# Performance work log

Hardware: AMD Instinct MI355X
Metric: run time of the kernel (lower is better)

The kernel has to match this reference:

```python
import jax, jax.numpy as jnp
import numpy as np
import math

GAMMA = 0.9
H = 8
SCALE_BASE = 512
TWO_PI = 2.0 * math.pi


def fixed_pos_embedding(scale):
    # scale: (L, d2) ; returns sin, cos of shape (L, d2)
    L, d2 = scale.shape
    inv_freq = 1.0 / (10000.0 ** (jnp.arange(d2, dtype=jnp.float32) / d2))
    sinusoid = jnp.arange(L, dtype=jnp.float32)[:, None] * inv_freq[None, :]
    return jnp.sin(sinusoid), jnp.cos(sinusoid)


def duplicate_interleave(m):
    # (L, d2) -> (L, 2*d2), each element duplicated along last axis
    return jnp.repeat(m, 2, axis=1)


def rotate_every_two(x):
    x1 = x[..., 0::2]
    x2 = x[..., 1::2]
    return jnp.stack([-x2, x1], axis=-1).reshape(x.shape)


def xpos(x, downscale=False):
    # x: (B, L, D) ; xpos rotary scaling (RetNet style, head_dim = D)
    B, L, D = x.shape
    base = (jnp.arange(0, D, 2, dtype=jnp.float32) + 0.4 * D) / (1.4 * D)  # (D/2,)
    power = (jnp.arange(L, dtype=jnp.float32) / SCALE_BASE)[:, None]       # (L, 1)
    scale = base[None, :] ** power                                          # (L, D/2)
    sin, cos = fixed_pos_embedding(scale)
    if downscale:
        scale = 1.0 / scale
    sin = duplicate_interleave(sin * scale)  # (L, D)
    cos = duplicate_interleave(cos * scale)  # (L, D)
    return x * cos[None] + rotate_every_two(x) * sin[None]


def pos_embed_sine(x, mask):
    # 1D DETR-style sine positional embedding. x: (B, L, D), mask: (1, L)
    D = x.shape[-1]
    x_embed = jnp.cumsum(mask, axis=1)
    x_embed = x_embed / (x_embed[:, -1:] + 1e-6) * TWO_PI
    dim_t = jnp.arange(D, dtype=jnp.float32)
    dim_t = 10000.0 ** (2.0 * jnp.floor(dim_t / 2.0) / D)
    pos = x_embed[:, :, None] / dim_t                       # (1, L, D)
    pos = jnp.stack([jnp.sin(pos[:, :, 0::2]), jnp.cos(pos[:, :, 1::2])], axis=3)
    return pos.reshape(1, x.shape[1], D)


def _split_heads(x):
    # (B, S, D) -> (B*H, S, d_k), matching torch view(S, B*H, d_k).transpose(0,1)
    B, S, D = x.shape
    return x.transpose(1, 0, 2).reshape(S, B * H, D // H).transpose(1, 0, 2)


def _forward(src, W_txt_Q, W_txt_K, W_txt_V, W_vid_Q, W_vid_K, W_vid_V,
             learn_vid_ret, W_out, b_out, row_idx, col_idx, txt_len):
    B, S, Dm = src.shape
    vid_len = S - txt_len
    dk = Dm // H
    # retention decay matrix D (lower triangular gamma^(n-m))
    n = jnp.arange(S)[:, None]
    m = jnp.arange(S)[None, :]
    expo = jnp.where(n >= m, n - m, 0).astype(jnp.float32)
    Dmat = jnp.where(n >= m, GAMMA ** expo, 0.0)
    # learned sparse mask: gather-expanded (vid_len,vid_len) table -> (S,S)
    temp = learn_vid_ret.reshape(vid_len, vid_len)
    learn_ret = jax.nn.sigmoid(temp[row_idx, col_idx])  # (S, S)
    diag = jnp.eye(S, dtype=src.dtype)
    video_ret = (1.0 - diag) * learn_ret
    learn_mask = diag + video_ret
    mask = Dmat * learn_mask   # mask_mode='both'
    loss_sparsity = jnp.mean(jnp.abs(video_ret))
    # projections (att_mode='all')
    txt = src[:, :txt_len]
    vid = src[:, txt_len:]
    mask_txt = jnp.ones((1, txt_len), dtype=src.dtype)
    pos = pos_embed_sine(txt, mask_txt)
    txt_Q = (pos + txt) @ W_txt_Q
    txt_K = (pos + txt) @ W_txt_K
    txt_V = txt @ W_txt_V
    vid_Q = xpos(vid) @ W_vid_Q
    vid_K = xpos(vid, downscale=True) @ W_vid_K
    vid_V = vid @ W_vid_V
    Q = jnp.concatenate([txt_Q, vid_Q], axis=1)
    K = jnp.concatenate([txt_K, vid_K], axis=1)
    V = jnp.concatenate([txt_V, vid_V], axis=1)
    q = _split_heads(Q) / math.sqrt(dk)   # (B*H, S, dk)
    k = _split_heads(K)
    v = _split_heads(V)
    attn = jnp.einsum('bqd,bkd->bqk', q, k) * mask[None]  # multiplicative mask pre-softmax
    attn = jax.nn.softmax(attn, axis=-1)
    ctx = jnp.einsum('bqk,bkd->bqd', attn, v)             # (B*H, S, dk)
    ctx = ctx.transpose(1, 0, 2).reshape(S, B, Dm)
    out = ctx @ W_out.T + b_out                            # output Linear
    out = out.transpose(1, 0, 2)                           # (B, S, Dm)
    att = attn.reshape(B, H, S, S).sum(axis=1) / H
    return out, att, loss_sparsity


def setup_inputs() -> dict:
    key = jax.random.key(0)
    ks = jax.random.split(key, 12)
    B, S, Dm, txt_len = 16, 1056, 256, 32
    vid_len = S - txt_len
    inp = {
        'src': jax.random.normal(ks[0], (B, S, Dm), dtype=jnp.float32),
        'W_txt_Q': jax.random.normal(ks[1], (Dm, Dm), dtype=jnp.float32) / Dm,
        'W_txt_K': jax.random.normal(ks[2], (Dm, Dm), dtype=jnp.float32) / Dm,
        'W_txt_V': jax.random.normal(ks[3], (Dm, Dm), dtype=jnp.float32) / Dm,
        'W_vid_Q': jax.random.normal(ks[4], (Dm, Dm), dtype=jnp.float32) / Dm,
        'W_vid_K': jax.random.normal(ks[5], (Dm, Dm), dtype=jnp.float32) / Dm,
        'W_vid_V': jax.random.normal(ks[6], (Dm, Dm), dtype=jnp.float32) / Dm,
        'learn_vid_ret': jax.random.normal(ks[7], (vid_len * vid_len, 1), dtype=jnp.float32),
        'W_out': jax.random.normal(ks[8], (Dm, Dm), dtype=jnp.float32) / math.sqrt(Dm),
        'b_out': jnp.zeros((Dm,), dtype=jnp.float32),
        'row_idx': jax.random.randint(ks[9], (S, S), 0, vid_len, dtype=jnp.int32),
        'col_idx': jax.random.randint(ks[10], (S, S), 0, vid_len, dtype=jnp.int32),
        'txt_len': txt_len,
    }
    return inp


def reference(src, W_txt_Q, W_txt_K, W_txt_V, W_vid_Q, W_vid_K, W_vid_V,
              learn_vid_ret, W_out, b_out, row_idx, col_idx, txt_len):
    return _forward(src, W_txt_Q, W_txt_K, W_txt_V, W_vid_Q, W_vid_K, W_vid_V,
                    learn_vid_ret, W_out, b_out, row_idx, col_idx, txt_len)
```

## Files before the change

kernel.cpp:

```cpp
#include <hip/hip_runtime.h>
#include <math.h>

#define B_   16
#define S_   1056
#define DM_  256
#define H_   8
#define DK_  32
#define TXT_ 32
#define VID_ 1024
#define SS_  (S_*S_)
#define NQT_ 66
#define NKT_ 66
#define MASK_BLKS 1089

#define LOG2_10000f 13.28771237954945f
#define LOG2_GAMMAf (-0.15200309344504995f)
#define RSQRT_DKf   0.17677669529663687f
#define TWO_PIf     6.283185307179586f
#define LOG2Ef      1.4426950408889634f

typedef __attribute__((ext_vector_type(8))) short bf16x8;
typedef __attribute__((ext_vector_type(4))) short bf16x4;
typedef __attribute__((ext_vector_type(4))) float f32x4;

__device__ __forceinline__ short f2bf(float f){
    unsigned u = __float_as_uint(f);
    unsigned r = u + 0x7FFFu + ((u >> 16) & 1u);
    return (short)(r >> 16);
}
__device__ __forceinline__ float bf2f(unsigned short s){
    return __uint_as_float(((unsigned)s) << 16);
}
__device__ __forceinline__ float fexp2(float x){
#if __has_builtin(__builtin_amdgcn_exp2f)
    return __builtin_amdgcn_exp2f(x);
#else
    return exp2f(x);
#endif
}
__device__ __forceinline__ bf16x4 pack_bf16x4(float e0, float e1, float e2, float e3){
    unsigned w0, w1;
    asm("v_cvt_pk_bf16_f32 %0, %1, %2" : "=v"(w0) : "v"(e0), "v"(e1));
    asm("v_cvt_pk_bf16_f32 %0, %1, %2" : "=v"(w1) : "v"(e2), "v"(e3));
    uint2 u = make_uint2(w0, w1);
    return *(bf16x4*)&u;
}

__device__ __forceinline__ f32x4 mfma16(bf16x4 a, bf16x4 b, f32x4 c){
#if __has_builtin(__builtin_amdgcn_mfma_f32_16x16x16bf16_1k)
    return __builtin_amdgcn_mfma_f32_16x16x16bf16_1k(a, b, c, 0, 0, 0);
#else
    f32x4 d = c;
    asm("v_mfma_f32_16x16x16_bf16 %0, %1, %2, %0" : "+v"(d) : "v"(a), "v"(b));
    return d;
#endif
}

__global__ __launch_bounds__(256) void k_mask(const float* __restrict__ lvr,
                       const int* __restrict__ row_idx, const int* __restrict__ col_idx,
                       short* __restrict__ maskf, float* __restrict__ partials)
{
    int T  = blockIdx.x*256 + threadIdx.x;
    int l  = T & 63;
    int qk = T >> 6;
    int qt = qk / 66;
    int kt = qk - qt*66;
    int i  = qt*16 + (l & 15);
    int j0 = kt*16 + 4*(l >> 4);
    size_t idx = (size_t)i*S_ + j0;
    int4 ri4 = *(const int4*)&row_idx[idx];
    int4 ci4 = *(const int4*)&col_idx[idx];
    int rr[4] = {ri4.x, ri4.y, ri4.z, ri4.w};
    int cc[4] = {ci4.x, ci4.y, ci4.z, ci4.w};
    float vrs = 0.f;
    short4 mq;
    short* mp = (short*)&mq;
    #pragma unroll
    for (int jj = 0; jj < 4; ++jj) {
        int j = j0 + jj;
        float vr, lm;
        if (i == j) { vr = 0.f; lm = 1.f; }
        else {
            float t = lvr[(size_t)rr[jj]*VID_ + cc[jj]];
            float sg = 1.f/(1.f + expf(-t));
            vr = sg; lm = sg;
        }
        float dmat = (i >= j) ? exp2f((float)(i-j)*LOG2_GAMMAf) : 0.f;
        mp[jj] = f2bf(dmat * lm * LOG2Ef);
        vrs += vr;
    }
    *(short4*)&maskf[(size_t)qk*256 + l*4] = mq;

    float s = vrs;
    #pragma unroll
    for (int m=1; m<64; m<<=1) s += __shfl_xor(s, m, 64);
    __shared__ float ws4[4];
    if ((threadIdx.x & 63) == 0) ws4[threadIdx.x>>6] = s;
    __syncthreads();
    if (threadIdx.x == 0) partials[blockIdx.x] = ws4[0]+ws4[1]+ws4[2]+ws4[3];
}

__global__ __launch_bounds__(256) void k_loss(const float* __restrict__ partials,
                                              float* __restrict__ out_loss)
{
    float s = 0.f;
    for (int i = threadIdx.x; i < MASK_BLKS; i += 256) s += partials[i];
    #pragma unroll
    for (int m=1; m<64; m<<=1) s += __shfl_xor(s, m, 64);
    __shared__ float ws4[4];
    if ((threadIdx.x & 63) == 0) ws4[threadIdx.x>>6] = s;
    __syncthreads();
    if (threadIdx.x == 0) out_loss[0] = (ws4[0]+ws4[1]+ws4[2]+ws4[3]) * (1.f/(float)SS_);
}

__global__ __launch_bounds__(256) void k_wprep(
    const float* __restrict__ Wtq, const float* __restrict__ Wtk, const float* __restrict__ Wtv,
    const float* __restrict__ Wvq, const float* __restrict__ Wvk, const float* __restrict__ Wvv,
    const float* __restrict__ Wout, short* __restrict__ Wf, short* __restrict__ WoF)
{
    int seg = blockIdx.x >> 8;
    int r   = blockIdx.x & 255;
    int tid = threadIdx.x;
    int tb16 = r >> 4, lr = r & 15;
    int kk = tid >> 5, lg = (tid >> 3) & 3, j = tid & 7;
    size_t off = (((size_t)tb16*8 + kk) << 9) + (lr + 16*lg)*8 + j;
    if (seg == 6) {
        WoF[off] = f2bf(Wout[r*256 + tid]);
    } else {
        const float* Wsrc = seg==0?Wtq: seg==1?Wtk: seg==2?Wtv: seg==3?Wvq: seg==4?Wvk: Wvv;
        Wf[((size_t)seg << 16) + off] = f2bf(Wsrc[tid*256 + r]);
    }
}

__global__ __launch_bounds__(256, 2) void k_qkv(const float* __restrict__ src,
    const short* __restrict__ WFq, const short* __restrict__ WFk, const short* __restrict__ WFv,
    short* __restrict__ Qb, short* __restrict__ Kf, short* __restrict__ Vf, int is_txt)
{
    __shared__ __align__(16) short xb[3][16][256];
    __shared__ float invf[128];
    __shared__ float lbs[128];
    int tid = threadIdx.x;
    int r0 = blockIdx.x * 16;
    int b, srow0;
    if (is_txt) { b = r0 >> 5;  srow0 = r0 & 31; }
    else        { b = r0 >> 10; srow0 = TXT_ + (r0 & 1023); }
    int t16 = srow0 >> 4;

    if (tid < 128) {
        float fk = (float)tid;
        invf[tid] = exp2f(-fk*(1.f/128.f)*LOG2_10000f);
        lbs[tid]  = log2f((2.f*fk + 102.4f) * (1.f/358.4f));
    }
    __syncthreads();

    #pragma unroll
    for (int it = 0; it < 8; ++it) {
        int task = it*256 + tid;
        int k  = task >> 4;
        int rr = task & 15;
        int srow = srow0 + rr;
        float2 x01 = ((const float2*)(src + ((size_t)b*S_ + srow)*DM_))[k];
        float a0, a1, c0, c1;
        if (is_txt) {
            float xe  = (float)(srow + 1) * (TWO_PIf/(32.f + 1e-6f));
            float arg = xe * invf[k];
            float sn = __sinf(arg), cs = __cosf(arg);
            a0 = x01.x + sn; a1 = x01.y + cs;
            c0 = a0; c1 = a1;
        } else {
            int l = srow - TXT_;
            float arg = (float)l * invf[k];
            float sn = __sinf(arg), cs = __cosf(arg);
            float scale = exp2f((float)l*(1.f/512.f)*lbs[k]);
            float rsc = 1.f/scale;
            float y0 = x01.x*cs - x01.y*sn;
            float y1 = x01.y*cs + x01.x*sn;
            a0 = y0*scale; a1 = y1*scale;
            c0 = y0*rsc;   c1 = y1*rsc;
        }
        int col = (2*k) ^ ((rr&7)<<3);
        *(short2*)&xb[0][rr][col] = make_short2(f2bf(a0), f2bf(a1));
        *(short2*)&xb[1][rr][col] = make_short2(f2bf(c0), f2bf(c1));
        *(short2*)&xb[2][rr][col] = make_short2(f2bf(x01.x), f2bf(x01.y));
    }
    __syncthreads();

    int lane = tid & 63;
    int w    = tid >> 6;
    int lr   = lane & 15;
    int lg   = lane >> 4;
    int swzl = (lr & 7) << 3;

    const short* WFs[3] = {WFq, WFk, WFv};
    #pragma unroll
    for (int m = 0; m < 3; ++m) {
        bf16x8 xf[8];
        #pragma unroll
        for (int kk = 0; kk < 8; ++kk)
            xf[kk] = *(const bf16x8*)&xb[m][lr][(kk*32 + lg*8) ^ swzl];
        #pragma unroll
        for (int ct = 0; ct < 4; ++ct) {
            int tb16 = w + ct*4;
            int tb   = tb16 * 16;
            const short* Wp = WFs[m] + (((size_t)tb16*8) << 9) + lane*8;
            f32x4 acc = {0.f,0.f,0.f,0.f};
            if (m < 2) {
                #pragma unroll
                for (int kk = 0; kk < 8; ++kk) {
                    bf16x8 wf = *(const bf16x8*)(Wp + (kk << 9));
                    acc = __builtin_amdgcn_mfma_f32_16x16x32_bf16(wf, xf[kk], acc, 0, 0, 0);
                }
                int h  = tb >> 5;
                int d0 = (tb & 31) + lg*4;
                short4 s4;
                if (m == 0) {
                    s4.x=f2bf(acc[0]*RSQRT_DKf); s4.y=f2bf(acc[1]*RSQRT_DKf);
                    s4.z=f2bf(acc[2]*RSQRT_DKf); s4.w=f2bf(acc[3]*RSQRT_DKf);
                    size_t off = ((size_t)(b*H_+h)*S_ + srow0+lr)*DK_ + d0;
                    *(short4*)&Qb[off] = s4;
                } else {
                    s4.x=f2bf(acc[0]); s4.y=f2bf(acc[1]);
                    s4.z=f2bf(acc[2]); s4.w=f2bf(acc[3]);
                    int lK = lr + 16*(d0 >> 3);
                    *(short4*)&Kf[((((size_t)(b*H_+h)*NKT_ + t16) << 9)) + lK*8 + (d0 & 7)] = s4;
                }
            } else {
                #pragma unroll
                for (int kk = 0; kk < 8; ++kk) {
                    bf16x8 wf = *(const bf16x8*)(Wp + (kk << 9));
                    acc = __builtin_amdgcn_mfma_f32_16x16x32_bf16(xf[kk], wf, acc, 0, 0, 0);
                }
                int o = tb + lr;
                int h = o >> 5;
                int dh = (tb >> 4) & 1;
                short4 s4;
                s4.x=f2bf(acc[0]); s4.y=f2bf(acc[1]);
                s4.z=f2bf(acc[2]); s4.w=f2bf(acc[3]);
                *(short4*)&Vf[((((size_t)(b*H_+h)*NKT_ + t16)) << 9) + lane*8 + dh*4] = s4;
            }
        }
    }
}

#define CTX_TILE2(KF, M0V, M1V, VV)                                               \
    {                                                                             \
        f32x4 acc0 = {0.f,0.f,0.f,0.f};                                           \
        acc0 = __builtin_amdgcn_mfma_f32_16x16x32_bf16(KF, qf0, acc0, 0, 0, 0);   \
        f32x4 acc1 = {0.f,0.f,0.f,0.f};                                           \
        acc1 = __builtin_amdgcn_mfma_f32_16x16x32_bf16(KF, qf1, acc1, 0, 0, 0);   \
        float e0 = fexp2(acc0[0]*bf2f(M0V.x));                                    \
        float e1 = fexp2(acc0[1]*bf2f(M0V.y));                                    \
        float e2 = fexp2(acc0[2]*bf2f(M0V.z));                                    \
        float e3 = fexp2(acc0[3]*bf2f(M0V.w));                                    \
        rssum0 += (e0+e1) + (e2+e3);                                              \
        bf16x4 pb0 = pack_bf16x4(e0, e1, e2, e3);                                 \
        float f0 = fexp2(acc1[0]*bf2f(M1V.x));                                    \
        float f1 = fexp2(acc1[1]*bf2f(M1V.y));                                    \
        float f2 = fexp2(acc1[2]*bf2f(M1V.z));                                    \
        float f3 = fexp2(acc1[3]*bf2f(M1V.w));                                    \
        rssum1 += (f0+f1) + (f2+f3);                                              \
        bf16x4 pb1 = pack_bf16x4(f0, f1, f2, f3);                                 \
        bf16x4 vlo; vlo[0]=VV[0]; vlo[1]=VV[1]; vlo[2]=VV[2]; vlo[3]=VV[3];       \
        bf16x4 vhi; vhi[0]=VV[4]; vhi[1]=VV[5]; vhi[2]=VV[6]; vhi[3]=VV[7];       \
        pv00 = mfma16(pb0, vlo, pv00);                                            \
        pv01 = mfma16(pb0, vhi, pv01);                                            \
        pv10 = mfma16(pb1, vlo, pv10);                                            \
        pv11 = mfma16(pb1, vhi, pv11);                                            \
    }

__global__ __launch_bounds__(256, 4) void k_ctx(const short* __restrict__ Qb,
    const short* __restrict__ Kf, const short* __restrict__ Vf,
    const short* __restrict__ maskf, short* __restrict__ ctxf, float* __restrict__ denomG)
{
    int tid  = threadIdx.x;
    int lane = tid & 63;
    int w    = tid >> 6;
    int b    = blockIdx.x & 15;
    int qh   = blockIdx.x >> 4;
    int qt32 = qh >> 1;
    int head = (qh & 1)*4 + w;
    int q0   = qt32 * 32;
    int lr   = lane & 15;
    int lg   = lane >> 4;

    const int bh = b*H_ + head;
    bf16x8 qf0 = *(const bf16x8*)(Qb + ((size_t)bh*S_ + q0 + lr)*DK_ + lg*8);
    bf16x8 qf1 = *(const bf16x8*)(Qb + ((size_t)bh*S_ + q0 + 16 + lr)*DK_ + lg*8);
    const short* Kp  = Kf + (((size_t)bh*NKT_) << 9) + lane*8;
    const short* Vp  = Vf + (((size_t)bh*NKT_) << 9) + lane*8;
    const short* Mp0 = maskf + (((size_t)(qt32*2  )*NKT_) << 8) + lane*4;
    const short* Mp1 = maskf + (((size_t)(qt32*2+1)*NKT_) << 8) + lane*4;

    float rssum0 = 0.f, rssum1 = 0.f;
    f32x4 pv00 = {0.f,0.f,0.f,0.f}, pv01 = {0.f,0.f,0.f,0.f};
    f32x4 pv10 = {0.f,0.f,0.f,0.f}, pv11 = {0.f,0.f,0.f,0.f};

    for (int g = 0; g < 22; ++g) {
        int tb = g * 3;
        bf16x8 K[3], VV[3]; ushort4 M0[3], M1[3];
        #pragma unroll
        for (int c = 0; c < 3; ++c) {
            int t = tb + c;
            K[c]  = *(const bf16x8*)(Kp + (unsigned)t*512);
            VV[c] = *(const bf16x8*)(Vp + (unsigned)t*512);
            M0[c] = *(const ushort4*)(Mp0 + (unsigned)t*256);
            M1[c] = *(const ushort4*)(Mp1 + (unsigned)t*256);
        }
        #pragma unroll
        for (int c = 0; c < 3; ++c) {
            CTX_TILE2(K[c], M0[c], M1[c], VV[c])
        }
    }

    rssum0 += __shfl_xor(rssum0, 16, 64);
    rssum0 += __shfl_xor(rssum0, 32, 64);
    rssum1 += __shfl_xor(rssum1, 16, 64);
    rssum1 += __shfl_xor(rssum1, 32, 64);
    float rd0 = 1.f / rssum0;
    float rd1 = 1.f / rssum1;
    if (lane < 16) {
        denomG[(size_t)bh*S_ + q0 + lane]      = rd0;
        denomG[(size_t)bh*S_ + q0 + 16 + lane] = rd1;
    }

    size_t baseA = ((((size_t)b*NQT_ + qt32*2    )*8 + head) << 9);
    size_t baseB = ((((size_t)b*NQT_ + qt32*2 + 1)*8 + head) << 9);
    int j   = lr & 7;
    int lgl = lr >> 3;
    #pragma unroll
    for (int r = 0; r < 4; ++r) {
        float rdq0 = __shfl(rd0, 4*lg + r, 64);
        float rdq1 = __shfl(rd1, 4*lg + r, 64);
        int qm = 4*lg + r;
        ctxf[baseA + (qm + 16*lgl    )*8 + j] = f2bf(pv00[r] * rdq0);
        ctxf[baseA + (qm + 16*(2+lgl))*8 + j] = f2bf(pv01[r] * rdq0);
        ctxf[baseB + (qm + 16*lgl    )*8 + j] = f2bf(pv10[r] * rdq1);
        ctxf[baseB + (qm + 16*(2+lgl))*8 + j] = f2bf(pv11[r] * rdq1);
    }
}

__global__ __launch_bounds__(256, 4) void k_att(const short* __restrict__ Qb,
    const short* __restrict__ Kf, const short* __restrict__ maskf,
    const float* __restrict__ denomG, float* __restrict__ att)
{
    int tid  = threadIdx.x;
    int lane = tid & 63;
    int w    = tid >> 6;
    int b    = blockIdx.x & 15;
    int qt   = blockIdx.x >> 4;
    int q0   = qt * 16;
    int lr   = lane & 15;
    int lg   = lane >> 4;

    float rdv[8];
    #pragma unroll
    for (int h = 0; h < 8; ++h)
        rdv[h] = denomG[(size_t)(b*H_+h)*S_ + q0 + lr] * 0.125f;

    bf16x8 qf[8];
    #pragma unroll
    for (int h = 0; h < 8; ++h)
        qf[h] = *(const bf16x8*)(Qb + ((size_t)(b*H_+h)*S_ + q0+lr)*DK_ + lg*8);

    int nt = (w < 2) ? 17 : 16;
    for (int t = 0; t < nt; ++t) {
        int kt = t*4 + w;
        int k0 = kt*16;
        bf16x8 kf[8];
        #pragma unroll
        for (int h = 0; h < 8; ++h)
            kf[h] = *(const bf16x8*)(Kf + (((size_t)(b*H_+h)*NKT_ + kt) << 9) + lane*8);
        ushort4 mq = *(const ushort4*)(maskf + (((size_t)qt*NKT_ + kt) << 8) + lane*4);
        float m0 = bf2f(mq.x), m1 = bf2f(mq.y), m2 = bf2f(mq.z), m3 = bf2f(mq.w);
        f32x4 a = {0.f,0.f,0.f,0.f};
        #pragma unroll
        for (int h = 0; h < 8; ++h) {
            f32x4 s = {0.f,0.f,0.f,0.f};
            s = __builtin_amdgcn_mfma_f32_16x16x32_bf16(kf[h], qf[h], s, 0, 0, 0);
            a[0] = fmaf(fexp2(s[0]*m0), rdv[h], a[0]);
            a[1] = fmaf(fexp2(s[1]*m1), rdv[h], a[1]);
            a[2] = fmaf(fexp2(s[2]*m2), rdv[h], a[2]);
            a[3] = fmaf(fexp2(s[3]*m3), rdv[h], a[3]);
        }
        float4 o4 = make_float4(a[0], a[1], a[2], a[3]);
        *(float4*)&att[((size_t)b*S_ + q0+lr)*S_ + k0 + 4*lg] = o4;
    }
}

__global__ __launch_bounds__(256, 2) void k_outproj(const short* __restrict__ ctxf,
    const short* __restrict__ WoF, const float* __restrict__ bias, float* __restrict__ out)
{
    int tid  = threadIdx.x;
    int lane = tid & 63;
    int w    = tid >> 6;
    int lr   = lane & 15;
    int lg   = lane >> 4;
    int r0   = blockIdx.x * 16;

    bf16x8 cf[8];
    #pragma unroll
    for (int kk = 0; kk < 8; ++kk)
        cf[kk] = *(const bf16x8*)(ctxf + (((size_t)blockIdx.x*8 + kk) << 9) + lane*8);

    #pragma unroll
    for (int ct = 0; ct < 4; ++ct) {
        int tb16 = w + ct*4;
        int tb   = tb16 * 16;
        f32x4 acc = {0.f,0.f,0.f,0.f};
        #pragma unroll
        for (int kk = 0; kk < 8; ++kk) {
            bf16x8 wf = *(const bf16x8*)(WoF + (((size_t)tb16*8 + kk) << 9) + lane*8);
            acc = __builtin_amdgcn_mfma_f32_16x16x32_bf16(wf, cf[kk], acc, 0, 0, 0);
        }
        float4 b4 = *(const float4*)&bias[tb + lg*4];
        float4 o4 = make_float4(acc[0]+b4.x, acc[1]+b4.y, acc[2]+b4.z, acc[3]+b4.w);
        *(float4*)&out[(size_t)(r0+lr)*DM_ + tb + lg*4] = o4;
    }
}

extern "C" void kernel_launch(void* const* d_in, const int* in_sizes, int n_in,
                              void* d_out, int out_size, void* d_ws, size_t ws_size,
                              hipStream_t stream)
{
    (void)in_sizes; (void)n_in; (void)out_size; (void)ws_size;
    const float* src  = (const float*)d_in[0];
    const float* Wtq  = (const float*)d_in[1];
    const float* Wtk  = (const float*)d_in[2];
    const float* Wtv  = (const float*)d_in[3];
    const float* Wvq  = (const float*)d_in[4];
    const float* Wvk  = (const float*)d_in[5];
    const float* Wvv  = (const float*)d_in[6];
    const float* lvr  = (const float*)d_in[7];
    const float* Wout = (const float*)d_in[8];
    const float* bout = (const float*)d_in[9];
    const int*   rid  = (const int*)d_in[10];
    const int*   cid  = (const int*)d_in[11];

    const size_t QKV_SH = (size_t)B_*H_*S_*DK_;
    const size_t KF_SH  = (size_t)B_*H_*NKT_*512;
    const size_t VF_SH  = (size_t)B_*H_*NKT_*512;
    const size_t CTX_SH = (size_t)B_*S_*DM_;

    float* ws       = (float*)d_ws;
    float* partials = ws;
    float* denomG   = partials + MASK_BLKS;
    short* maskf    = (short*)(denomG + (size_t)B_*H_*S_);
    short* Qb       = maskf + SS_;
    short* Kf       = Qb + QKV_SH;
    short* Vf       = Kf + KF_SH;
    short* ctxf     = Vf + VF_SH;
    short* Wf       = ctxf + CTX_SH;
    short* WoF      = Wf + 6*65536;

    float* out  = (float*)d_out;
    float* att  = out + (size_t)B_*S_*DM_;
    float* loss = att + (size_t)B_*S_*S_;

    k_mask<<<MASK_BLKS, 256, 0, stream>>>(lvr, rid, cid, maskf, partials);
    k_wprep<<<7*256, 256, 0, stream>>>(Wtq, Wtk, Wtv, Wvq, Wvk, Wvv, Wout, Wf, WoF);
    k_qkv<<<(B_*TXT_)/16, 256, 0, stream>>>(src, Wf, Wf+65536, Wf+2*65536,
                                            Qb, Kf, Vf, 1);
    k_qkv<<<(B_*VID_)/16, 256, 0, stream>>>(src, Wf+3*65536, Wf+4*65536, Wf+5*65536,
                                            Qb, Kf, Vf, 0);
    k_ctx<<<B_*NQT_, 256, 0, stream>>>(Qb, Kf, Vf, maskf, ctxf, denomG);
    k_att<<<B_*NQT_, 256, 0, stream>>>(Qb, Kf, maskf, denomG, att);
    k_outproj<<<(B_*S_)/16, 256, 0, stream>>>(ctxf, WoF, bout, out);
    k_loss<<<1, 256, 0, stream>>>(partials, loss);
}
```

Measured before the change: 171.1 us.

## Widen ctx query tile to 48 rows and transpose att output for coalesced stores

The context kernel now handles 48 query rows per block (three 16-row tiles) instead of 32. Each K/V tile load is reused across more queries, at the cost of more registers and fewer blocks in the grid (704 instead of 1056). The attention-output kernel swaps the MFMA operand order so each lane writes consecutive key columns, which coalesces the large fp32 att stores. To support that, the mask kernel writes a second, transposed mask layout, which adds extra workspace and scattered 2-byte writes.

```diff
diff --git a/kernel.cpp b/kernel.cpp
--- a/kernel.cpp
+++ b/kernel.cpp
@@ -11,6 +11,7 @@
 #define SS_  (S_*S_)
 #define NQT_ 66
 #define NKT_ 66
+#define NQ48_ 22
 #define MASK_BLKS 1089
 
 #define LOG2_10000f 13.28771237954945f
@@ -58,7 +59,8 @@
 
 __global__ __launch_bounds__(256) void k_mask(const float* __restrict__ lvr,
                        const int* __restrict__ row_idx, const int* __restrict__ col_idx,
-                       short* __restrict__ maskf, float* __restrict__ partials)
+                       short* __restrict__ maskf, short* __restrict__ maskg,
+                       float* __restrict__ partials)
 {
     int T  = blockIdx.x*256 + threadIdx.x;
     int l  = T & 63;
@@ -90,6 +92,16 @@
         vrs += vr;
     }
     *(short4*)&maskf[(size_t)qk*256 + l*4] = mq;
+    {
+        int lq = l & 15;
+        int r2 = lq & 3;
+        int baseq = (lq >> 2) << 4;
+        #pragma unroll
+        for (int jj = 0; jj < 4; ++jj) {
+            int lanep = 4*(l >> 4) + jj + baseq;
+            maskg[(size_t)qk*256 + lanep*4 + r2] = mp[jj];
+        }
+    }
 
     float s = vrs;
     #pragma unroll
@@ -242,33 +254,43 @@
     }
 }
 
-#define CTX_TILE2(KF, M0V, M1V, VV)                                               \
-    {                                                                             \
-        f32x4 acc0 = {0.f,0.f,0.f,0.f};                                           \
-        acc0 = __builtin_amdgcn_mfma_f32_16x16x32_bf16(KF, qf0, acc0, 0, 0, 0);   \
-        f32x4 acc1 = {0.f,0.f,0.f,0.f};                                           \
-        acc1 = __builtin_amdgcn_mfma_f32_16x16x32_bf16(KF, qf1, acc1, 0, 0, 0);   \
-        float e0 = fexp2(acc0[0]*bf2f(M0V.x));                                    \
-        float e1 = fexp2(acc0[1]*bf2f(M0V.y));                                    \
-        float e2 = fexp2(acc0[2]*bf2f(M0V.z));                                    \
-        float e3 = fexp2(acc0[3]*bf2f(M0V.w));                                    \
-        rssum0 += (e0+e1) + (e2+e3);                                              \
-        bf16x4 pb0 = pack_bf16x4(e0, e1, e2, e3);                                 \
-        float f0 = fexp2(acc1[0]*bf2f(M1V.x));                                    \
-        float f1 = fexp2(acc1[1]*bf2f(M1V.y));                                    \
-        float f2 = fexp2(acc1[2]*bf2f(M1V.z));                                    \
-        float f3 = fexp2(acc1[3]*bf2f(M1V.w));                                    \
-        rssum1 += (f0+f1) + (f2+f3);                                              \
-        bf16x4 pb1 = pack_bf16x4(f0, f1, f2, f3);                                 \
-        bf16x4 vlo; vlo[0]=VV[0]; vlo[1]=VV[1]; vlo[2]=VV[2]; vlo[3]=VV[3];       \
-        bf16x4 vhi; vhi[0]=VV[4]; vhi[1]=VV[5]; vhi[2]=VV[6]; vhi[3]=VV[7];       \
-        pv00 = mfma16(pb0, vlo, pv00);                                            \
-        pv01 = mfma16(pb0, vhi, pv01);                                            \
-        pv10 = mfma16(pb1, vlo, pv10);                                            \
-        pv11 = mfma16(pb1, vhi, pv11);                                            \
-    }
-
-__global__ __launch_bounds__(256, 4) void k_ctx(const short* __restrict__ Qb,
+#define CTX_TILE3(KF, M0V, M1V, M2V, VV)                                           \
+    {                                                                              \
+        f32x4 acc0 = {0.f,0.f,0.f,0.f};                                            \
+        acc0 = __builtin_amdgcn_mfma_f32_16x16x32_bf16(KF, qf0, acc0, 0, 0, 0);    \
+        f32x4 acc1 = {0.f,0.f,0.f,0.f};                                            \
+        acc1 = __builtin_amdgcn_mfma_f32_16x16x32_bf16(KF, qf1, acc1, 0, 0, 0);    \
+        f32x4 acc2 = {0.f,0.f,0.f,0.f};                                            \
+        acc2 = __builtin_amdgcn_mfma_f32_16x16x32_bf16(KF, qf2, acc2, 0, 0, 0);    \
+        float e0 = fexp2(acc0[0]*bf2f(M0V.x));                                     \
+        float e1 = fexp2(acc0[1]*bf2f(M0V.y));                                     \
+        float e2 = fexp2(acc0[2]*bf2f(M0V.z));                                     \
+        float e3 = fexp2(acc0[3]*bf2f(M0V.w));                                     \
+        rssum0 += (e0+e1) + (e2+e3);                                               \
+        bf16x4 pb0 = pack_bf16x4(e0, e1, e2, e3);                                  \
+        float f0 = fexp2(acc1[0]*bf2f(M1V.x));                                     \
+        float f1 = fexp2(acc1[1]*bf2f(M1V.y));                                     \
+        float f2 = fexp2(acc1[2]*bf2f(M1V.z));                                     \
+        float f3 = fexp2(acc1[3]*bf2f(M1V.w));                                     \
+        rssum1 += (f0+f1) + (f2+f3);                                               \
+        bf16x4 pb1 = pack_bf16x4(f0, f1, f2, f3);                                  \
+        float g0 = fexp2(acc2[0]*bf2f(M2V.x));                                     \
+        float g1 = fexp2(acc2[1]*bf2f(M2V.y));                                     \
+        float g2 = fexp2(acc2[2]*bf2f(M2V.z));                                     \
+        float g3 = fexp2(acc2[3]*bf2f(M2V.w));                                     \
+        rssum2 += (g0+g1) + (g2+g3);                                               \
+        bf16x4 pb2 = pack_bf16x4(g0, g1, g2, g3);                                  \
+        bf16x4 vlo; vlo[0]=VV[0]; vlo[1]=VV[1]; vlo[2]=VV[2]; vlo[3]=VV[3];        \
+        bf16x4 vhi; vhi[0]=VV[4]; vhi[1]=VV[5]; vhi[2]=VV[6]; vhi[3]=VV[7];        \
+        pv00 = mfma16(pb0, vlo, pv00);                                             \
+        pv01 = mfma16(pb0, vhi, pv01);                                             \
+        pv10 = mfma16(pb1, vlo, pv10);                                             \
+        pv11 = mfma16(pb1, vhi, pv11);                                             \
+        pv20 = mfma16(pb2, vlo, pv20);                                             \
+        pv21 = mfma16(pb2, vhi, pv21);                                             \
+    }
+
+__global__ __launch_bounds__(256, 3) void k_ctx(const short* __restrict__ Qb,
     const short* __restrict__ Kf, const short* __restrict__ Vf,
     const short* __restrict__ maskf, short* __restrict__ ctxf, float* __restrict__ denomG)
 {
@@ -277,38 +299,42 @@
     int w    = tid >> 6;
     int b    = blockIdx.x & 15;
     int qh   = blockIdx.x >> 4;
-    int qt32 = qh >> 1;
+    int qt48 = qh >> 1;
     int head = (qh & 1)*4 + w;
-    int q0   = qt32 * 32;
+    int q0   = qt48 * 48;
     int lr   = lane & 15;
     int lg   = lane >> 4;
 
     const int bh = b*H_ + head;
-    bf16x8 qf0 = *(const bf16x8*)(Qb + ((size_t)bh*S_ + q0 + lr)*DK_ + lg*8);
+    bf16x8 qf0 = *(const bf16x8*)(Qb + ((size_t)bh*S_ + q0      + lr)*DK_ + lg*8);
     bf16x8 qf1 = *(const bf16x8*)(Qb + ((size_t)bh*S_ + q0 + 16 + lr)*DK_ + lg*8);
+    bf16x8 qf2 = *(const bf16x8*)(Qb + ((size_t)bh*S_ + q0 + 32 + lr)*DK_ + lg*8);
     const short* Kp  = Kf + (((size_t)bh*NKT_) << 9) + lane*8;
     const short* Vp  = Vf + (((size_t)bh*NKT_) << 9) + lane*8;
-    const short* Mp0 = maskf + (((size_t)(qt32*2  )*NKT_) << 8) + lane*4;
-    const short* Mp1 = maskf + (((size_t)(qt32*2+1)*NKT_) << 8) + lane*4;
-
-    float rssum0 = 0.f, rssum1 = 0.f;
+    const short* Mp0 = maskf + (((size_t)(qt48*3    )*NKT_) << 8) + lane*4;
+    const short* Mp1 = maskf + (((size_t)(qt48*3 + 1)*NKT_) << 8) + lane*4;
+    const short* Mp2 = maskf + (((size_t)(qt48*3 + 2)*NKT_) << 8) + lane*4;
+
+    float rssum0 = 0.f, rssum1 = 0.f, rssum2 = 0.f;
     f32x4 pv00 = {0.f,0.f,0.f,0.f}, pv01 = {0.f,0.f,0.f,0.f};
     f32x4 pv10 = {0.f,0.f,0.f,0.f}, pv11 = {0.f,0.f,0.f,0.f};
-
-    for (int g = 0; g < 22; ++g) {
-        int tb = g * 3;
-        bf16x8 K[3], VV[3]; ushort4 M0[3], M1[3];
-        #pragma unroll
-        for (int c = 0; c < 3; ++c) {
+    f32x4 pv20 = {0.f,0.f,0.f,0.f}, pv21 = {0.f,0.f,0.f,0.f};
+
+    for (int g = 0; g < 33; ++g) {
+        int tb = g * 2;
+        bf16x8 K[2], VV[2]; ushort4 M0[2], M1[2], M2[2];
+        #pragma unroll
+        for (int c = 0; c < 2; ++c) {
             int t = tb + c;
             K[c]  = *(const bf16x8*)(Kp + (unsigned)t*512);
             VV[c] = *(const bf16x8*)(Vp + (unsigned)t*512);
             M0[c] = *(const ushort4*)(Mp0 + (unsigned)t*256);
             M1[c] = *(const ushort4*)(Mp1 + (unsigned)t*256);
-        }
-        #pragma unroll
-        for (int c = 0; c < 3; ++c) {
-            CTX_TILE2(K[c], M0[c], M1[c], VV[c])
+            M2[c] = *(const ushort4*)(Mp2 + (unsigned)t*256);
+        }
+        #pragma unroll
+        for (int c = 0; c < 2; ++c) {
+            CTX_TILE3(K[c], M0[c], M1[c], M2[c], VV[c])
         }
     }
 
@@ -316,31 +342,39 @@
     rssum0 += __shfl_xor(rssum0, 32, 64);
     rssum1 += __shfl_xor(rssum1, 16, 64);
     rssum1 += __shfl_xor(rssum1, 32, 64);
+    rssum2 += __shfl_xor(rssum2, 16, 64);
+    rssum2 += __shfl_xor(rssum2, 32, 64);
     float rd0 = 1.f / rssum0;
     float rd1 = 1.f / rssum1;
+    float rd2 = 1.f / rssum2;
     if (lane < 16) {
-        denomG[(size_t)bh*S_ + q0 + lane]      = rd0;
+        denomG[(size_t)bh*S_ + q0      + lane] = rd0;
         denomG[(size_t)bh*S_ + q0 + 16 + lane] = rd1;
-    }
-
-    size_t baseA = ((((size_t)b*NQT_ + qt32*2    )*8 + head) << 9);
-    size_t baseB = ((((size_t)b*NQT_ + qt32*2 + 1)*8 + head) << 9);
+        denomG[(size_t)bh*S_ + q0 + 32 + lane] = rd2;
+    }
+
+    size_t baseA = ((((size_t)b*NQT_ + qt48*3    )*8 + head) << 9);
+    size_t baseB = ((((size_t)b*NQT_ + qt48*3 + 1)*8 + head) << 9);
+    size_t baseC = ((((size_t)b*NQT_ + qt48*3 + 2)*8 + head) << 9);
     int j   = lr & 7;
     int lgl = lr >> 3;
     #pragma unroll
     for (int r = 0; r < 4; ++r) {
         float rdq0 = __shfl(rd0, 4*lg + r, 64);
         float rdq1 = __shfl(rd1, 4*lg + r, 64);
+        float rdq2 = __shfl(rd2, 4*lg + r, 64);
         int qm = 4*lg + r;
         ctxf[baseA + (qm + 16*lgl    )*8 + j] = f2bf(pv00[r] * rdq0);
         ctxf[baseA + (qm + 16*(2+lgl))*8 + j] = f2bf(pv01[r] * rdq0);
         ctxf[baseB + (qm + 16*lgl    )*8 + j] = f2bf(pv10[r] * rdq1);
         ctxf[baseB + (qm + 16*(2+lgl))*8 + j] = f2bf(pv11[r] * rdq1);
+        ctxf[baseC + (qm + 16*lgl    )*8 + j] = f2bf(pv20[r] * rdq2);
+        ctxf[baseC + (qm + 16*(2+lgl))*8 + j] = f2bf(pv21[r] * rdq2);
     }
 }
 
 __global__ __launch_bounds__(256, 4) void k_att(const short* __restrict__ Qb,
-    const short* __restrict__ Kf, const short* __restrict__ maskf,
+    const short* __restrict__ Kf, const short* __restrict__ maskg,
     const float* __restrict__ denomG, float* __restrict__ att)
 {
     int tid  = threadIdx.x;
@@ -352,10 +386,12 @@
     int lr   = lane & 15;
     int lg   = lane >> 4;
 
-    float rdv[8];
-    #pragma unroll
-    for (int h = 0; h < 8; ++h)
-        rdv[h] = denomG[(size_t)(b*H_+h)*S_ + q0 + lr] * 0.125f;
+    float4 rdv[8];
+    #pragma unroll
+    for (int h = 0; h < 8; ++h) {
+        float4 v = *(const float4*)&denomG[(size_t)(b*H_+h)*S_ + q0 + 4*lg];
+        rdv[h] = make_float4(v.x*0.125f, v.y*0.125f, v.z*0.125f, v.w*0.125f);
+    }
 
     bf16x8 qf[8];
     #pragma unroll
@@ -370,20 +406,21 @@
         #pragma unroll
         for (int h = 0; h < 8; ++h)
             kf[h] = *(const bf16x8*)(Kf + (((size_t)(b*H_+h)*NKT_ + kt) << 9) + lane*8);
-        ushort4 mq = *(const ushort4*)(maskf + (((size_t)qt*NKT_ + kt) << 8) + lane*4);
+        ushort4 mq = *(const ushort4*)(maskg + (((size_t)qt*NKT_ + kt) << 8) + lane*4);
         float m0 = bf2f(mq.x), m1 = bf2f(mq.y), m2 = bf2f(mq.z), m3 = bf2f(mq.w);
         f32x4 a = {0.f,0.f,0.f,0.f};
         #pragma unroll
         for (int h = 0; h < 8; ++h) {
             f32x4 s = {0.f,0.f,0.f,0.f};
-            s = __builtin_amdgcn_mfma_f32_16x16x32_bf16(kf[h], qf[h], s, 0, 0, 0);
-            a[0] = fmaf(fexp2(s[0]*m0), rdv[h], a[0]);
-            a[1] = fmaf(fexp2(s[1]*m1), rdv[h], a[1]);
-            a[2] = fmaf(fexp2(s[2]*m2), rdv[h], a[2]);
-            a[3] = fmaf(fexp2(s[3]*m3), rdv[h], a[3]);
-        }
-        float4 o4 = make_float4(a[0], a[1], a[2], a[3]);
-        *(float4*)&att[((size_t)b*S_ + q0+lr)*S_ + k0 + 4*lg] = o4;
+            s = __builtin_amdgcn_mfma_f32_16x16x32_bf16(qf[h], kf[h], s, 0, 0, 0);
+            a[0] = fmaf(fexp2(s[0]*m0), rdv[h].x, a[0]);
+            a[1] = fmaf(fexp2(s[1]*m1), rdv[h].y, a[1]);
+            a[2] = fmaf(fexp2(s[2]*m2), rdv[h].z, a[2]);
+            a[3] = fmaf(fexp2(s[3]*m3), rdv[h].w, a[3]);
+        }
+        #pragma unroll
+        for (int r = 0; r < 4; ++r)
+            att[((size_t)b*S_ + q0 + 4*lg + r)*S_ + k0 + lr] = a[r];
     }
 }
 
@@ -445,7 +482,8 @@
     float* partials = ws;
     float* denomG   = partials + MASK_BLKS;
     short* maskf    = (short*)(denomG + (size_t)B_*H_*S_);
-    short* Qb       = maskf + SS_;
+    short* maskg    = maskf + SS_;
+    short* Qb       = maskg + SS_;
     short* Kf       = Qb + QKV_SH;
     short* Vf       = Kf + KF_SH;
     short* ctxf     = Vf + VF_SH;
@@ -456,14 +494,14 @@
     float* att  = out + (size_t)B_*S_*DM_;
     float* loss = att + (size_t)B_*S_*S_;
 
-    k_mask<<<MASK_BLKS, 256, 0, stream>>>(lvr, rid, cid, maskf, partials);
+    k_mask<<<MASK_BLKS, 256, 0, stream>>>(lvr, rid, cid, maskf, maskg, partials);
     k_wprep<<<7*256, 256, 0, stream>>>(Wtq, Wtk, Wtv, Wvq, Wvk, Wvv, Wout, Wf, WoF);
     k_qkv<<<(B_*TXT_)/16, 256, 0, stream>>>(src, Wf, Wf+65536, Wf+2*65536,
                                             Qb, Kf, Vf, 1);
     k_qkv<<<(B_*VID_)/16, 256, 0, stream>>>(src, Wf+3*65536, Wf+4*65536, Wf+5*65536,
                                             Qb, Kf, Vf, 0);
-    k_ctx<<<B_*NQT_, 256, 0, stream>>>(Qb, Kf, Vf, maskf, ctxf, denomG);
-    k_att<<<B_*NQT_, 256, 0, stream>>>(Qb, Kf, maskf, denomG, att);
+    k_ctx<<<B_*NQ48_*2, 256, 0, stream>>>(Qb, Kf, Vf, maskf, ctxf, denomG);
+    k_att<<<B_*NQT_, 256, 0, stream>>>(Qb, Kf, maskg, denomG, att);
     k_outproj<<<(B_*S_)/16, 256, 0, stream>>>(ctxf, WoF, bout, out);
     k_loss<<<1, 256, 0, stream>>>(partials, loss);
 }
```

New measurement: 158.6 us. -7.3%, faster.
